# Optimization experiments

Hardware: AMD Instinct MI355X
Metric: run time of the kernel (lower is better)

Reference implementation:

```python
import jax, jax.numpy as jnp
import numpy as np

B, Q, K = 4, 256, 1024
Q_SIZE, K_SIZE, V_SIZE, H = 256, 256, 256, 128
NEG = -1000000.0


def setup_inputs() -> dict:
    key = jax.random.key(0)
    ks = jax.random.split(key, 7)
    return {
        "queries": jax.random.normal(ks[0], (B, Q, Q_SIZE), dtype=jnp.float32),
        "keys": jax.random.normal(ks[1], (B, K, K_SIZE), dtype=jnp.float32),
        "values": jax.random.normal(ks[2], (B, K, V_SIZE), dtype=jnp.float32),
        "valid_lens": jax.random.randint(ks[3], (B,), 1, K + 1),
        # Linear weights stored torch-style: [out_features, in_features]
        "W_q": jax.random.normal(ks[4], (H, Q_SIZE), dtype=jnp.float32) * (1.0 / np.sqrt(Q_SIZE)),
        "W_k": jax.random.normal(ks[5], (H, K_SIZE), dtype=jnp.float32) * (1.0 / np.sqrt(K_SIZE)),
        "w_v": jax.random.normal(ks[6], (H,), dtype=jnp.float32) * (1.0 / np.sqrt(H)),
    }


def reference(queries, keys, values, valid_lens, W_q, W_k, w_v):
    # Projections (torch Linear: x @ W.T)
    q = jnp.einsum("bqi,hi->bqh", queries, W_q)  # [B,Q,H]
    k = jnp.einsum("bki,hi->bkh", keys, W_k)     # [B,K,H]
    # Broadcast add + tanh -> additive scores via dot with w_v
    feat = jnp.tanh(q[:, :, None, :] + k[:, None, :, :])  # [B,Q,K,H]
    scores = jnp.einsum("bqkh,h->bqk", feat, w_v)          # [B,Q,K]
    # masked_softmax: 1-D valid_lens broadcast over all query rows
    mask = jnp.arange(K)[None, None, :] < valid_lens[:, None, None]  # [B,1,K]
    scores = jnp.where(mask, scores, NEG)
    attn = jax.nn.softmax(scores, axis=-1)
    # dropout p=0.0 (eval): identity
    return jnp.einsum("bqk,bkv->bqv", attn, values)  # [B,Q,V]
```

## Files before the change

### kernel.cpp

```cpp
#include <hip/hip_runtime.h>
#include <math.h>

#define BQ   4
#define QN   256
#define KN   1024
#define DIN  256
#define HD   128

#define C2F   2.8853900817779268f
#define NL2E  (-2.8853900817779268f)

__global__ __launch_bounds__(256, 2) void proj_kernel(const float* __restrict__ queries,
                                                      const float* __restrict__ keys,
                                                      const float* __restrict__ W_q,
                                                      const float* __restrict__ W_k,
                                                      float* __restrict__ Eq,
                                                      float* __restrict__ EkT4) {
    __shared__ float xT[32][36];
    __shared__ float WT[32][136];

    const int t = threadIdx.x;
    const int row0 = blockIdx.x * 32;
    const bool is_q = row0 < BQ * QN;
    const float* x = is_q ? queries : keys;
    const float* W = is_q ? W_q : W_k;
    const int xr0 = is_q ? row0 : row0 - BQ * QN;

    const int h0 = (t & 31) * 4;
    const int r0 = (t >> 5) * 4;

    float acc[4][4];
#pragma unroll
    for (int r = 0; r < 4; r++)
#pragma unroll
        for (int c = 0; c < 4; c++) acc[r][c] = 0.f;

    for (int ks = 0; ks < DIN; ks += 32) {
        __syncthreads();
        {
            const int r = t >> 3, k4 = (t & 7) * 4;
            float4 xv = *(const float4*)(x + (size_t)(xr0 + r) * DIN + ks + k4);
            xT[k4 + 0][r] = xv.x; xT[k4 + 1][r] = xv.y;
            xT[k4 + 2][r] = xv.z; xT[k4 + 3][r] = xv.w;
        }
#pragma unroll
        for (int u = 0; u < 4; u++) {
            const int h = (t >> 3) + 32 * u, k4 = (t & 7) * 4;
            float4 wv = *(const float4*)(W + (size_t)h * DIN + ks + k4);
            WT[k4 + 0][h] = wv.x; WT[k4 + 1][h] = wv.y;
            WT[k4 + 2][h] = wv.z; WT[k4 + 3][h] = wv.w;
        }
        __syncthreads();
#pragma unroll
        for (int kk = 0; kk < 32; kk++) {
            float4 xv = *(const float4*)&xT[kk][r0];
            float4 wv = *(const float4*)&WT[kk][h0];
            const float xr[4] = {xv.x, xv.y, xv.z, xv.w};
            const float wc[4] = {wv.x, wv.y, wv.z, wv.w};
#pragma unroll
            for (int r = 0; r < 4; r++)
#pragma unroll
                for (int c = 0; c < 4; c++)
                    acc[r][c] = __builtin_fmaf(xr[r], wc[c], acc[r][c]);
        }
    }

    if (is_q) {
#pragma unroll
        for (int r = 0; r < 4; r++) {
            float4 o;
            o.x = __builtin_amdgcn_exp2f(C2F * acc[r][0]);
            o.y = __builtin_amdgcn_exp2f(C2F * acc[r][1]);
            o.z = __builtin_amdgcn_exp2f(C2F * acc[r][2]);
            o.w = __builtin_amdgcn_exp2f(C2F * acc[r][3]);
            *(float4*)(Eq + (size_t)(row0 + r0 + r) * HD + h0) = o;
        }
    } else {
        const int krow = row0 - BQ * QN;
        const int b = krow >> 10, k0 = (krow & (KN - 1)) + r0;
        const int h4 = t & 31;
        float* base = EkT4 + ((size_t)(b * 32 + h4) * KN + k0) * 4;
#pragma unroll
        for (int r = 0; r < 4; r++) {
            float4 o;
            o.x = __builtin_amdgcn_exp2f(C2F * acc[r][0]);
            o.y = __builtin_amdgcn_exp2f(C2F * acc[r][1]);
            o.z = __builtin_amdgcn_exp2f(C2F * acc[r][2]);
            o.w = __builtin_amdgcn_exp2f(C2F * acc[r][3]);
            *(float4*)(base + (size_t)r * 4) = o;
        }
    }
}

__global__ __launch_bounds__(256, 4) void score_kernel(const float* __restrict__ Eq,
                                                       const float* __restrict__ EkT4,
                                                       const int* __restrict__ valid_lens,
                                                       const float* __restrict__ w_v,
                                                       float* __restrict__ attn,
                                                       float* __restrict__ partial) {
    __shared__ float s_w[HD];
    __shared__ float s_pq[HD][8];
    __shared__ float s_part[2][8][128];
    __shared__ float s_red[4][4];

    const int blk = blockIdx.x;
    const int b = blk & 3;
    const int q0 = ((blk >> 2) & 31) * 8;
    const int c = blk >> 7;
    const int t = threadIdx.x;
    const int valid = valid_lens[b];
    float* pp = partial + (size_t)(b * QN + q0) * 8;

    if (c * 128 >= valid) {
        if (t < 8) pp[t * 8 + c] = 0.f;
        return;
    }

    const int kl = t & 127;
    const int hh = t >> 7;
    const int k = c * 128 + kl;

    if (t < HD) s_w[t] = w_v[t];
    {
        const int h = t & 127;
#pragma unroll
        for (int j = 0; j < 4; j++) {
            const int q = (t >> 7) * 4 + j;
            s_pq[h][q] = Eq[(size_t)(b * QN + q0 + q) * HD + h];
        }
    }
    __syncthreads();

    const float4* kcol = (const float4*)EkT4 + ((size_t)(b * 32 + hh * 16) * KN + k);
    float acc[8] = {0.f, 0.f, 0.f, 0.f, 0.f, 0.f, 0.f, 0.f};

#pragma unroll 4
    for (int i = 0; i < 16; i++) {
        float4 ek4 = kcol[(size_t)i * KN];
        const int hb = hh * 64 + i * 4;
        const float ekv[4] = {ek4.x, ek4.y, ek4.z, ek4.w};
#pragma unroll
        for (int j = 0; j < 4; j++) {
            const float ek = ekv[j];
            const float w = s_w[hb + j];
            float4 p0 = *(const float4*)&s_pq[hb + j][0];
            float4 p1 = *(const float4*)&s_pq[hb + j][4];
            acc[0] = __builtin_fmaf(w, __builtin_amdgcn_rcpf(__builtin_fmaf(ek, p0.x, 1.0f)), acc[0]);
            acc[1] = __builtin_fmaf(w, __builtin_amdgcn_rcpf(__builtin_fmaf(ek, p0.y, 1.0f)), acc[1]);
            acc[2] = __builtin_fmaf(w, __builtin_amdgcn_rcpf(__builtin_fmaf(ek, p0.z, 1.0f)), acc[2]);
            acc[3] = __builtin_fmaf(w, __builtin_amdgcn_rcpf(__builtin_fmaf(ek, p0.w, 1.0f)), acc[3]);
            acc[4] = __builtin_fmaf(w, __builtin_amdgcn_rcpf(__builtin_fmaf(ek, p1.x, 1.0f)), acc[4]);
            acc[5] = __builtin_fmaf(w, __builtin_amdgcn_rcpf(__builtin_fmaf(ek, p1.y, 1.0f)), acc[5]);
            acc[6] = __builtin_fmaf(w, __builtin_amdgcn_rcpf(__builtin_fmaf(ek, p1.z, 1.0f)), acc[6]);
            acc[7] = __builtin_fmaf(w, __builtin_amdgcn_rcpf(__builtin_fmaf(ek, p1.w, 1.0f)), acc[7]);
        }
    }

#pragma unroll
    for (int q = 0; q < 8; q++) s_part[hh][q][kl] = acc[q];
    __syncthreads();

    const int qb = (t >> 7) * 4;
    float* arow = attn + (size_t)(b * QN + q0 + qb) * KN + k;
    float psum[4];
#pragma unroll
    for (int j = 0; j < 4; j++) {
        const int q = qb + j;
        float tot = s_part[0][q][kl] + s_part[1][q][kl];
        float e = (k < valid) ? __builtin_amdgcn_exp2f(NL2E * tot) : 0.f;
        arow[(size_t)j * KN] = e;
#pragma unroll
        for (int off = 32; off > 0; off >>= 1) e += __shfl_xor(e, off, 64);
        psum[j] = e;
    }
    const int wv = t >> 6;
    if ((t & 63) == 0) {
#pragma unroll
        for (int j = 0; j < 4; j++) s_red[wv][j] = psum[j];
    }
    __syncthreads();
    if (t < 8) {
        const int q = t;
        float s = (q < 4) ? (s_red[0][q] + s_red[1][q])
                          : (s_red[2][q - 4] + s_red[3][q - 4]);
        pp[q * 8 + c] = s;
    }
}

__global__ __launch_bounds__(256, 2) void av_kernel(const float* __restrict__ attn,
                                                    const float* __restrict__ partial,
                                                    const float* __restrict__ values,
                                                    const int* __restrict__ valid_lens,
                                                    float* __restrict__ out) {
    __shared__ float s_e[2][8][68];
    __shared__ float s_part[2][8][68];

    const int blk = blockIdx.x;
    const int b = blk & 3;
    const int q0 = ((blk >> 2) & 31) * 8;
    const int vb = blk >> 7;
    const int t = threadIdx.x;
    const int ks = t >> 7;
    const int q = (t >> 4) & 7;
    const int vt = (t & 15) * 4;
    const int voff = vb * 64 + vt;
    const int valid = valid_lens[b];

    const int lim0 = min(valid, 512);
    const int T0 = (lim0 + 63) >> 6;
    const int myLim = ks ? max(0, valid - 512) : lim0;
    const int myBeg = ks * 512;

    const float* arow = attn + (size_t)(b * QN + q0 + q) * KN + myBeg + vt;
    const float* vp = values + (size_t)b * KN * DIN + voff;

    float4 acc = {0.f, 0.f, 0.f, 0.f};
    for (int it = 0; it < T0; it++) {
        const int kt = it * 64;
        const bool act = kt < myLim;
        __syncthreads();
        if (act)
            *(float4*)&s_e[ks][q][vt] = *(const float4*)(arow + kt);
        __syncthreads();
        if (act) {
            const float* vk = vp + (size_t)(myBeg + kt) * DIN;
#pragma unroll 4
            for (int kk = 0; kk < 64; kk += 4) {
                float4 aw = *(const float4*)&s_e[ks][q][kk];
                float4 v0 = *(const float4*)(vk + (size_t)kk * DIN);
                float4 v1 = *(const float4*)(vk + (size_t)(kk + 1) * DIN);
                float4 v2 = *(const float4*)(vk + (size_t)(kk + 2) * DIN);
                float4 v3 = *(const float4*)(vk + (size_t)(kk + 3) * DIN);
                acc.x += aw.x * v0.x + aw.y * v1.x + aw.z * v2.x + aw.w * v3.x;
                acc.y += aw.x * v0.y + aw.y * v1.y + aw.z * v2.y + aw.w * v3.y;
                acc.z += aw.x * v0.z + aw.y * v1.z + aw.z * v2.z + aw.w * v3.z;
                acc.w += aw.x * v0.w + aw.y * v1.w + aw.z * v2.w + aw.w * v3.w;
            }
        }
    }

    *(float4*)&s_part[ks][q][vt] = acc;
    __syncthreads();
    if (t < 128) {
        const int q2 = t >> 4, v4 = (t & 15) * 4;
        float4 a0 = *(const float4*)&s_part[0][q2][v4];
        float4 a1 = *(const float4*)&s_part[1][q2][v4];
        const float* pr = partial + (size_t)(b * QN + q0 + q2) * 8;
        float4 pA = *(const float4*)pr;
        float4 pB = *(const float4*)(pr + 4);
        const float inv = 1.0f / (pA.x + pA.y + pA.z + pA.w + pB.x + pB.y + pB.z + pB.w);
        float4 o;
        o.x = (a0.x + a1.x) * inv;
        o.y = (a0.y + a1.y) * inv;
        o.z = (a0.z + a1.z) * inv;
        o.w = (a0.w + a1.w) * inv;
        *(float4*)(out + (size_t)(b * QN + q0 + q2) * DIN + vb * 64 + v4) = o;
    }
}

extern "C" void kernel_launch(void* const* d_in, const int* in_sizes, int n_in,
                              void* d_out, int out_size, void* d_ws, size_t ws_size,
                              hipStream_t stream) {
    const float* queries    = (const float*)d_in[0];
    const float* keys       = (const float*)d_in[1];
    const float* values     = (const float*)d_in[2];
    const int*   valid_lens = (const int*)d_in[3];
    const float* W_q        = (const float*)d_in[4];
    const float* W_k        = (const float*)d_in[5];
    const float* w_v        = (const float*)d_in[6];
    float* out = (float*)d_out;

    float* Eq      = (float*)d_ws;
    float* EkT4    = Eq + (size_t)BQ * QN * HD;
    float* attn    = EkT4 + (size_t)BQ * HD * KN;
    float* partial = attn + (size_t)BQ * QN * KN;

    proj_kernel<<<(BQ * QN + BQ * KN) / 32, 256, 0, stream>>>(queries, keys, W_q, W_k, Eq, EkT4);
    score_kernel<<<BQ * (QN / 8) * 8, 256, 0, stream>>>(Eq, EkT4, valid_lens, w_v, attn, partial);
    av_kernel<<<BQ * (QN / 8) * 4, 256, 0, stream>>>(attn, partial, values, valid_lens, out);
}
```

Before: 127.9 us.

## Retile attention-value GEMM into 32x32 register-blocked tiles; halve projection tile rows

The attention-times-values kernel changes from per-row streaming of values out of global memory to a 32x32 output tile. Each tile stages attention (transposed) and value slabs in shared memory with register prefetch, uses a 4x4 register micro-tile, and splits K four ways with a shared-memory reduction. The aim is reuse of each value load across 32 query rows, where the old layout re-read values for every 8-query block. The projection kernel drops from 32 to 16 rows per block, doubling the block count for better occupancy at the cost of less reuse of W. The new av_kernel has one K-split per wavefront with a smaller grid, 256 blocks, which may underfill the GPU.

Measured after the change: 112.9 us. -11.7%, faster.

```diff
diff --git a/kernel.cpp b/kernel.cpp
--- a/kernel.cpp
+++ b/kernel.cpp
@@ -16,28 +16,28 @@
                                                       const float* __restrict__ W_k,
                                                       float* __restrict__ Eq,
                                                       float* __restrict__ EkT4) {
-    __shared__ float xT[32][36];
+    __shared__ float xT[32][18];
     __shared__ float WT[32][136];
 
     const int t = threadIdx.x;
-    const int row0 = blockIdx.x * 32;
+    const int row0 = blockIdx.x * 16;
     const bool is_q = row0 < BQ * QN;
     const float* x = is_q ? queries : keys;
     const float* W = is_q ? W_q : W_k;
     const int xr0 = is_q ? row0 : row0 - BQ * QN;
 
     const int h0 = (t & 31) * 4;
-    const int r0 = (t >> 5) * 4;
-
-    float acc[4][4];
-#pragma unroll
-    for (int r = 0; r < 4; r++)
+    const int r0 = (t >> 5) * 2;
+
+    float acc[2][4];
+#pragma unroll
+    for (int r = 0; r < 2; r++)
 #pragma unroll
         for (int c = 0; c < 4; c++) acc[r][c] = 0.f;
 
     for (int ks = 0; ks < DIN; ks += 32) {
         __syncthreads();
-        {
+        if (t < 128) {
             const int r = t >> 3, k4 = (t & 7) * 4;
             float4 xv = *(const float4*)(x + (size_t)(xr0 + r) * DIN + ks + k4);
             xT[k4 + 0][r] = xv.x; xT[k4 + 1][r] = xv.y;
@@ -53,12 +53,12 @@
         __syncthreads();
 #pragma unroll
         for (int kk = 0; kk < 32; kk++) {
-            float4 xv = *(const float4*)&xT[kk][r0];
+            float2 xv = *(const float2*)&xT[kk][r0];
             float4 wv = *(const float4*)&WT[kk][h0];
-            const float xr[4] = {xv.x, xv.y, xv.z, xv.w};
+            const float xr[2] = {xv.x, xv.y};
             const float wc[4] = {wv.x, wv.y, wv.z, wv.w};
 #pragma unroll
-            for (int r = 0; r < 4; r++)
+            for (int r = 0; r < 2; r++)
 #pragma unroll
                 for (int c = 0; c < 4; c++)
                     acc[r][c] = __builtin_fmaf(xr[r], wc[c], acc[r][c]);
@@ -67,7 +67,7 @@
 
     if (is_q) {
 #pragma unroll
-        for (int r = 0; r < 4; r++) {
+        for (int r = 0; r < 2; r++) {
             float4 o;
             o.x = __builtin_amdgcn_exp2f(C2F * acc[r][0]);
             o.y = __builtin_amdgcn_exp2f(C2F * acc[r][1]);
@@ -79,15 +79,14 @@
         const int krow = row0 - BQ * QN;
         const int b = krow >> 10, k0 = (krow & (KN - 1)) + r0;
         const int h4 = t & 31;
-        float* base = EkT4 + ((size_t)(b * 32 + h4) * KN + k0) * 4;
-#pragma unroll
-        for (int r = 0; r < 4; r++) {
+#pragma unroll
+        for (int r = 0; r < 2; r++) {
             float4 o;
             o.x = __builtin_amdgcn_exp2f(C2F * acc[r][0]);
             o.y = __builtin_amdgcn_exp2f(C2F * acc[r][1]);
             o.z = __builtin_amdgcn_exp2f(C2F * acc[r][2]);
             o.w = __builtin_amdgcn_exp2f(C2F * acc[r][3]);
-            *(float4*)(base + (size_t)r * 4) = o;
+            *(float4*)(EkT4 + ((size_t)(b * 32 + h4) * KN + k0 + r) * 4) = o;
         }
     }
 }
@@ -192,69 +191,88 @@
                                                     const float* __restrict__ values,
                                                     const int* __restrict__ valid_lens,
                                                     float* __restrict__ out) {
-    __shared__ float s_e[2][8][68];
-    __shared__ float s_part[2][8][68];
+    __shared__ float s_aT[32][36];
+    __shared__ float s_v[32][36];
+    __shared__ float s_red[4][32][36];
+    __shared__ float s_inv[32];
 
     const int blk = blockIdx.x;
     const int b = blk & 3;
-    const int q0 = ((blk >> 2) & 31) * 8;
-    const int vb = blk >> 7;
+    const int qt = (blk >> 2) & 7;
+    const int vt = blk >> 5;
     const int t = threadIdx.x;
-    const int ks = t >> 7;
-    const int q = (t >> 4) & 7;
-    const int vt = (t & 15) * 4;
-    const int voff = vb * 64 + vt;
+    const int q0 = qt * 32, v0 = vt * 32;
     const int valid = valid_lens[b];
-
-    const int lim0 = min(valid, 512);
-    const int T0 = (lim0 + 63) >> 6;
-    const int myLim = ks ? max(0, valid - 512) : lim0;
-    const int myBeg = ks * 512;
-
-    const float* arow = attn + (size_t)(b * QN + q0 + q) * KN + myBeg + vt;
-    const float* vp = values + (size_t)b * KN * DIN + voff;
-
-    float4 acc = {0.f, 0.f, 0.f, 0.f};
-    for (int it = 0; it < T0; it++) {
-        const int kt = it * 64;
-        const bool act = kt < myLim;
-        __syncthreads();
-        if (act)
-            *(float4*)&s_e[ks][q][vt] = *(const float4*)(arow + kt);
-        __syncthreads();
-        if (act) {
-            const float* vk = vp + (size_t)(myBeg + kt) * DIN;
-#pragma unroll 4
-            for (int kk = 0; kk < 64; kk += 4) {
-                float4 aw = *(const float4*)&s_e[ks][q][kk];
-                float4 v0 = *(const float4*)(vk + (size_t)kk * DIN);
-                float4 v1 = *(const float4*)(vk + (size_t)(kk + 1) * DIN);
-                float4 v2 = *(const float4*)(vk + (size_t)(kk + 2) * DIN);
-                float4 v3 = *(const float4*)(vk + (size_t)(kk + 3) * DIN);
-                acc.x += aw.x * v0.x + aw.y * v1.x + aw.z * v2.x + aw.w * v3.x;
-                acc.y += aw.x * v0.y + aw.y * v1.y + aw.z * v2.y + aw.w * v3.y;
-                acc.z += aw.x * v0.z + aw.y * v1.z + aw.z * v2.z + aw.w * v3.z;
-                acc.w += aw.x * v0.w + aw.y * v1.w + aw.z * v2.w + aw.w * v3.w;
-            }
-        }
-    }
-
-    *(float4*)&s_part[ks][q][vt] = acc;
-    __syncthreads();
-    if (t < 128) {
-        const int q2 = t >> 4, v4 = (t & 15) * 4;
-        float4 a0 = *(const float4*)&s_part[0][q2][v4];
-        float4 a1 = *(const float4*)&s_part[1][q2][v4];
-        const float* pr = partial + (size_t)(b * QN + q0 + q2) * 8;
+    const int T = (valid + 31) >> 5;
+
+    if (t < 32) {
+        const float* pr = partial + (size_t)(b * QN + q0 + t) * 8;
         float4 pA = *(const float4*)pr;
         float4 pB = *(const float4*)(pr + 4);
-        const float inv = 1.0f / (pA.x + pA.y + pA.z + pA.w + pB.x + pB.y + pB.z + pB.w);
+        s_inv[t] = 1.0f / (pA.x + pA.y + pA.z + pA.w + pB.x + pB.y + pB.z + pB.w);
+    }
+
+    const int sr = t >> 3, sc = (t & 7) * 4;
+    const float* abase = attn + (size_t)(b * QN + q0 + sr) * KN + sc;
+    const float* vbase = values + ((size_t)b * KN + sr) * DIN + v0 + sc;
+
+    const int vh = t & 7, qh = (t >> 3) & 7, ks = t >> 6;
+
+    float acc[4][4];
+#pragma unroll
+    for (int r = 0; r < 4; r++)
+#pragma unroll
+        for (int c = 0; c < 4; c++) acc[r][c] = 0.f;
+
+    float4 ra = *(const float4*)abase;
+    float4 rv = *(const float4*)vbase;
+
+    for (int tile = 0; tile < T; tile++) {
+        __syncthreads();
+        s_aT[sc + 0][sr] = ra.x;
+        s_aT[sc + 1][sr] = ra.y;
+        s_aT[sc + 2][sr] = ra.z;
+        s_aT[sc + 3][sr] = ra.w;
+        *(float4*)&s_v[sr][sc] = rv;
+        __syncthreads();
+        if (tile + 1 < T) {
+            ra = *(const float4*)(abase + (tile + 1) * 32);
+            rv = *(const float4*)(vbase + (size_t)(tile + 1) * 32 * DIN);
+        }
+#pragma unroll
+        for (int i = 0; i < 8; i++) {
+            const int kk = ks * 8 + i;
+            float4 aq = *(const float4*)&s_aT[kk][qh * 4];
+            float4 vv = *(const float4*)&s_v[kk][vh * 4];
+            const float ar[4] = {aq.x, aq.y, aq.z, aq.w};
+            const float vc[4] = {vv.x, vv.y, vv.z, vv.w};
+#pragma unroll
+            for (int r = 0; r < 4; r++)
+#pragma unroll
+                for (int c = 0; c < 4; c++)
+                    acc[r][c] = __builtin_fmaf(ar[r], vc[c], acc[r][c]);
+        }
+    }
+
+#pragma unroll
+    for (int r = 0; r < 4; r++)
+        *(float4*)&s_red[ks][qh * 4 + r][vh * 4] =
+            make_float4(acc[r][0], acc[r][1], acc[r][2], acc[r][3]);
+    __syncthreads();
+
+    {
+        const int q = t >> 3, v4 = (t & 7) * 4;
+        float4 r0 = *(const float4*)&s_red[0][q][v4];
+        float4 r1 = *(const float4*)&s_red[1][q][v4];
+        float4 r2 = *(const float4*)&s_red[2][q][v4];
+        float4 r3 = *(const float4*)&s_red[3][q][v4];
+        const float inv = s_inv[q];
         float4 o;
-        o.x = (a0.x + a1.x) * inv;
-        o.y = (a0.y + a1.y) * inv;
-        o.z = (a0.z + a1.z) * inv;
-        o.w = (a0.w + a1.w) * inv;
-        *(float4*)(out + (size_t)(b * QN + q0 + q2) * DIN + vb * 64 + v4) = o;
+        o.x = (r0.x + r1.x + r2.x + r3.x) * inv;
+        o.y = (r0.y + r1.y + r2.y + r3.y) * inv;
+        o.z = (r0.z + r1.z + r2.z + r3.z) * inv;
+        o.w = (r0.w + r1.w + r2.w + r3.w) * inv;
+        *(float4*)(out + (size_t)(b * QN + q0 + q) * DIN + v0 + v4) = o;
     }
 }
 
@@ -275,7 +293,7 @@
     float* attn    = EkT4 + (size_t)BQ * HD * KN;
     float* partial = attn + (size_t)BQ * QN * KN;
 
-    proj_kernel<<<(BQ * QN + BQ * KN) / 32, 256, 0, stream>>>(queries, keys, W_q, W_k, Eq, EkT4);
+    proj_kernel<<<(BQ * QN + BQ * KN) / 16, 256, 0, stream>>>(queries, keys, W_q, W_k, Eq, EkT4);
     score_kernel<<<BQ * (QN / 8) * 8, 256, 0, stream>>>(Eq, EkT4, valid_lens, w_v, attn, partial);
-    av_kernel<<<BQ * (QN / 8) * 4, 256, 0, stream>>>(attn, partial, values, valid_lens, out);
-}
+    av_kernel<<<BQ * 8 * 8, 256, 0, stream>>>(attn, partial, values, valid_lens, out);
+}
```
